# Optimization experiments

Measured on AMD Instinct MI355X. Metric: run time of the kernel, lower is better.

## Reference

```python
import jax, jax.numpy as jnp
import numpy as np

LEVELS = 6
_S = float(1.0 / np.sqrt(2.0))  # forward transform scales kernels by 1/sqrt(2)
# Complex Daubechies 6-tap filters (real, imag), pre-scaled for the forward DWT.
LO_R = [v * _S for v in (-0.0662912607, 0.1104854346, 0.6629126074, 0.6629126074, 0.1104854346, -0.0662912607)]
LO_I = [v * _S for v in (-0.0855816496, -0.0855816496, 0.1711632992, 0.1711632992, -0.0855816496, -0.0855816496)]
HI_R = [v * _S for v in (-0.0662912607, -0.1104854346, 0.6629126074, -0.6629126074, 0.1104854346, 0.0662912607)]
HI_I = [v * _S for v in (0.0855816496, -0.0855816496, -0.1711632992, 0.1711632992, 0.0855816496, -0.0855816496)]


def _corr_down(v, k):
    """Circular-padded 6-tap correlation along last axis, stride-2 decimation.
    v: [..., L] (L even) -> [..., L//2]. Matches torch: circular pad 3 each side,
    valid conv (L+1 outputs), then slice 0:-1:2."""
    L = v.shape[-1]
    vp = jnp.concatenate([v[..., -3:], v, v[..., :3]], axis=-1)  # [..., L+6]
    out = k[0] * vp[..., 0:L - 1:2]
    for t in range(1, 6):
        out = out + k[t] * vp[..., t:t + L - 1:2]
    return out


def _cconv_down(xr, xi, kr, ki):
    """Complex conv + downsample: (xr + i*xi) * (kr + i*ki) along last axis."""
    return (_corr_down(xr, kr) - _corr_down(xi, ki),
            _corr_down(xr, ki) + _corr_down(xi, kr))


def _decompose(xr, xi):
    """One DWT level. xr, xi: [B, C, h, w] -> (zr, zi) same shape."""
    # vertical pass: convolve along h (transpose so h is last)
    xrT = xr.swapaxes(-1, -2)  # [B, C, w, h]
    xiT = xi.swapaxes(-1, -2)
    lr, li = _cconv_down(xrT, xiT, LO_R, LO_I)  # [B, C, w, h//2]
    hr, hi = _cconv_down(xrT, xiT, HI_R, HI_I)
    yr = jnp.concatenate([lr, hr], axis=-1).swapaxes(-1, -2)  # [B, C, h, w]
    yi = jnp.concatenate([li, hi], axis=-1).swapaxes(-1, -2)
    # horizontal pass: convolve along w
    lr, li = _cconv_down(yr, yi, LO_R, LO_I)  # [B, C, h, w//2]
    hr, hi = _cconv_down(yr, yi, HI_R, HI_I)
    zr = jnp.concatenate([lr, hr], axis=-1)
    zi = jnp.concatenate([li, hi], axis=-1)
    return zr, zi


def setup_inputs() -> dict:
    key = jax.random.key(0)
    images = jax.random.uniform(key, (8, 3, 1024, 1024), dtype=jnp.float32)
    return {"images": images}


def reference(images):
    B, C, H, W = images.shape
    xr = images
    xi = jnp.zeros_like(images)
    res_r = jnp.zeros((B, C, H, W), images.dtype)
    res_i = jnp.zeros((B, C, H, W), images.dtype)
    for i in range(LEVELS):
        h, w = H >> i, W >> i
        if i == 0:
            sr, si = xr, xi
        else:
            sr, si = res_r[..., :h, :w], res_i[..., :h, :w]
        dr, di = _decompose(sr, si)
        res_r = res_r.at[..., :h, :w].set(dr)
        res_i = res_i.at[..., :h, :w].set(di)
    return jnp.stack([res_r, res_i], axis=2)  # [B, C, 2, H, W]
```

## Files before the change

kernel.cpp:

```cpp
#include <hip/hip_runtime.h>


#define SQ2 0.7071067811865476

constexpr float kLOR0 = (float)(-0.0662912607 * SQ2);
constexpr float kLOR1 = (float)( 0.1104854346 * SQ2);
constexpr float kLOR2 = (float)( 0.6629126074 * SQ2);
constexpr float kLOI0 = (float)(-0.0855816496 * SQ2);
constexpr float kLOI1 = (float)(-0.0855816496 * SQ2);
constexpr float kLOI2 = (float)( 0.1711632992 * SQ2);
constexpr float kHIR0 = (float)(-0.0662912607 * SQ2);
constexpr float kHIR1 = (float)(-0.1104854346 * SQ2);
constexpr float kHIR2 = (float)( 0.6629126074 * SQ2);
constexpr float kHII0 = (float)( 0.0855816496 * SQ2);
constexpr float kHII1 = (float)(-0.0855816496 * SQ2);
constexpr float kHII2 = (float)(-0.1711632992 * SQ2);

typedef float f2v __attribute__((ext_vector_type(2)));

__device__ __forceinline__ void band6(const float* xr, const float* xi,
                                      float& plr, float& pli, float& phr,
                                      float& phi) {
  const float s0 = xr[0] + xr[5], s1 = xr[1] + xr[4], s2 = xr[2] + xr[3];
  const float d0 = xr[0] - xr[5], d1 = xr[1] - xr[4], d2 = xr[2] - xr[3];
  const float t0 = xi[0] + xi[5], t1 = xi[1] + xi[4], t2 = xi[2] + xi[3];
  const float e0 = xi[0] - xi[5], e1 = xi[1] - xi[4], e2 = xi[2] - xi[3];
  plr = (kLOR0 * s0 + kLOR1 * s1 + kLOR2 * s2) -
        (kLOI0 * t0 + kLOI1 * t1 + kLOI2 * t2);
  pli = (kLOI0 * s0 + kLOI1 * s1 + kLOI2 * s2) +
        (kLOR0 * t0 + kLOR1 * t1 + kLOR2 * t2);
  phr = (kHIR0 * d0 + kHIR1 * d1 + kHIR2 * d2) -
        (kHII0 * e0 + kHII1 * e1 + kHII2 * e2);
  phi = (kHII0 * d0 + kHII1 * d1 + kHII2 * d2) +
        (kHIR0 * e0 + kHIR1 * e1 + kHIR2 * e2);
}

template <int TB, bool HAS_IMAG, bool LL_TO_WS>
__global__ __launch_bounds__(256) void dwt_kernel(
    const float* __restrict__ inR, const float* __restrict__ inI,
    float* __restrict__ out, float* __restrict__ llR, float* __restrict__ llI,
    int h, int w, int tilesPerRow, int tilesPerPlane, int cpx8, int HW,
    int W0) {
  constexpr int RROWS = 2 * TB + 4;
  constexpr int F4PR = TB / 2 + 2;
  constexpr int SW = 4 * F4PR;
  constexpr int NF4 = RROWS * F4PR;
  constexpr int NF4P = ((NF4 + 255) / 256) * 256;
  constexpr int YW = 2 * TB + 5;
  constexpr int HB = TB / 2;

  __shared__ float4 s4R[NF4P];
  __shared__ float4 s4I[HAS_IMAG ? NF4P : 1];
  __shared__ float yLR[HB * YW], yLI[HB * YW], yHR[HB * YW], yHI[HB * YW];

  const int tid = threadIdx.x;
  int bid = (int)blockIdx.x;
  bid = (bid & 7) * cpx8 + (bid >> 3);
  const int plane = bid / tilesPerPlane;
  const int trem = bid - plane * tilesPerPlane;
  const int ti = trem / tilesPerRow;
  const int tj = trem - ti * tilesPerRow;

  const int hm = h - 1;
  const int w4 = w >> 2, w4m = w4 - 1;
  const int rowstart = 2 * TB * ti - 3;
  const int col4start = HB * tj - 1;

  const float* pinR = inR + (size_t)plane * h * w;
  const float* pinI = HAS_IMAG ? (inI + (size_t)plane * h * w) : nullptr;

  {
    const int lane = tid & 63;
    const int wid = tid >> 6;
    for (int c0 = wid * 64; c0 < NF4P; c0 += 256) {
      const int idx = c0 + lane;
      const int r = idx / F4PR;
      const int q = idx - r * F4PR;
      const int gr = (rowstart + r) & hm;
      const int gq = (col4start + q) & w4m;
      const size_t goff = (size_t)gr * w4 + gq;
      __builtin_amdgcn_global_load_lds(
          (__attribute__((address_space(1))) void*)((const float4*)pinR + goff),
          (__attribute__((address_space(3))) void*)(&s4R[c0]), 16, 0, 0);
      if (HAS_IMAG) {
        __builtin_amdgcn_global_load_lds(
            (__attribute__((address_space(1))) void*)((const float4*)pinI + goff),
            (__attribute__((address_space(3))) void*)(&s4I[c0]), 16, 0, 0);
      }
    }
  }
  __syncthreads();

  const float* sRf = (const float*)s4R;
  const float* sIf = (const float*)s4I;
  const int i0 = TB * ti, j0g = TB * tj;
  const int h2 = h >> 1, w2 = w >> 1;
  float* outR = out + (size_t)plane * 2 * HW;
  float* outI = outR + HW;

#pragma unroll
  for (int p = 0; p < 2; ++p) {
    for (int idx = tid; idx < HB * YW; idx += 256) {
      const int il = idx / YW;
      const int c = idx - il * YW;
      const int rb = 2 * (p * HB + il);
      const float* col = sRf + rb * SW + c;
      const float x0 = col[0], x1 = col[SW], x2 = col[2 * SW];
      const float x3 = col[3 * SW], x4 = col[4 * SW], x5 = col[5 * SW];
      const float sr0 = x0 + x5, sr1 = x1 + x4, sr2 = x2 + x3;
      const float dr0 = x0 - x5, dr1 = x1 - x4, dr2 = x2 - x3;
      float lr = kLOR0 * sr0 + kLOR1 * sr1 + kLOR2 * sr2;
      float li = kLOI0 * sr0 + kLOI1 * sr1 + kLOI2 * sr2;
      float hr = kHIR0 * dr0 + kHIR1 * dr1 + kHIR2 * dr2;
      float hi = kHII0 * dr0 + kHII1 * dr1 + kHII2 * dr2;
      if (HAS_IMAG) {
        const float* colI = sIf + rb * SW + c;
        const float z0 = colI[0], z1 = colI[SW], z2 = colI[2 * SW];
        const float z3 = colI[3 * SW], z4 = colI[4 * SW], z5 = colI[5 * SW];
        const float si0 = z0 + z5, si1 = z1 + z4, si2 = z2 + z3;
        const float di0 = z0 - z5, di1 = z1 - z4, di2 = z2 - z3;
        lr -= kLOI0 * si0 + kLOI1 * si1 + kLOI2 * si2;
        li += kLOR0 * si0 + kLOR1 * si1 + kLOR2 * si2;
        hr -= kHII0 * di0 + kHII1 * di1 + kHII2 * di2;
        hi += kHIR0 * di0 + kHIR1 * di1 + kHIR2 * di2;
      }
      yLR[idx] = lr;
      yLI[idx] = li;
      yHR[idx] = hr;
      yHI[idx] = hi;
    }
    __syncthreads();

    constexpr int NJQ = TB / 2;
    const int jq = tid & (NJQ - 1);
    const int il = tid / NJQ;
    if (il < HB) {
      float o[8][2];
#pragma unroll
      for (int u = 0; u < 2; ++u) {
        const int cb = il * YW + 4 * jq + 2 * u + 1;
        band6(&yLR[cb], &yLI[cb], o[0][u], o[1][u], o[2][u], o[3][u]);
        band6(&yHR[cb], &yHI[cb], o[4][u], o[5][u], o[6][u], o[7][u]);
      }
      const int gi = i0 + p * HB + il;
      const int gj = j0g + 2 * jq;
      const int rlo = gi, rhi = h2 + gi, clo = gj, chi = w2 + gj;
      auto st = [&](float* pdst, int v) {
        f2v t;
        t.x = o[v][0];
        t.y = o[v][1];
        __builtin_nontemporal_store(t, (f2v*)pdst);
      };
      st(outR + (size_t)rlo * W0 + chi, 2);
      st(outI + (size_t)rlo * W0 + chi, 3);
      st(outR + (size_t)rhi * W0 + clo, 4);
      st(outI + (size_t)rhi * W0 + clo, 5);
      st(outR + (size_t)rhi * W0 + chi, 6);
      st(outI + (size_t)rhi * W0 + chi, 7);
      if (LL_TO_WS) {
        const size_t off = (size_t)plane * h2 * w2 + (size_t)gi * w2 + gj;
        f2v a, b;
        a.x = o[0][0];
        a.y = o[0][1];
        b.x = o[1][0];
        b.y = o[1][1];
        *(f2v*)(llR + off) = a;
        *(f2v*)(llI + off) = b;
      } else {
        st(outR + (size_t)rlo * W0 + clo, 0);
        st(outI + (size_t)rlo * W0 + clo, 1);
      }
    }
    __syncthreads();
  }
}

extern "C" void kernel_launch(void* const* d_in, const int* in_sizes, int n_in,
                              void* d_out, int out_size, void* d_ws,
                              size_t ws_size, hipStream_t stream) {
  const float* images = (const float*)d_in[0];
  float* out = (float*)d_out;
  constexpr int B = 8, C = 3, H = 1024, W = 1024, LEVELS = 6;

  float* wsf = (float*)d_ws;
  const size_t S0 = (size_t)B * C * 512 * 512;
  const size_t S1 = (size_t)B * C * 256 * 256;
  float* buf0R = wsf;
  float* buf0I = wsf + S0;
  float* buf1R = wsf + 2 * S0;
  float* buf1I = wsf + 2 * S0 + S1;

  const float* curR = images;
  const float* curI = nullptr;

  for (int lvl = 0; lvl < LEVELS; ++lvl) {
    const int h = H >> lvl, w = W >> lvl;
    const int TBl = (lvl == 5) ? 16 : 32;
    const int tpr = (w / 2) / TBl;
    const int tpp = tpr * tpr;
    const int grid = B * C * tpp;
    const int cpx8 = grid / 8;
    float* llR = (lvl & 1) ? buf1R : buf0R;
    float* llI = (lvl & 1) ? buf1I : buf0I;

    if (lvl == 0) {
      dwt_kernel<32, false, true><<<grid, 256, 0, stream>>>(
          curR, nullptr, out, llR, llI, h, w, tpr, tpp, cpx8, H * W, W);
    } else if (lvl < LEVELS - 1) {
      dwt_kernel<32, true, true><<<grid, 256, 0, stream>>>(
          curR, curI, out, llR, llI, h, w, tpr, tpp, cpx8, H * W, W);
    } else {
      dwt_kernel<16, true, false><<<grid, 256, 0, stream>>>(
          curR, curI, out, nullptr, nullptr, h, w, tpr, tpp, cpx8, H * W, W);
    }
    curR = llR;
    curI = llI;
  }
}
```

Measured before the change: 99.58 us.

## Fuse last three DWT levels into one per-plane tail kernel; vectorize LDS reads

Replaces the three separate launches for the small levels (128, 64, 32) with one tail kernel where each block handles one plane and loops over all three levels and their tiles. Intermediate LL data goes through workspace between levels. This removes launch and tail-latency overhead for the small grids. It also pads the intermediate LDS rows so the horizontal pass loads its inputs with aligned float4 reads instead of scalar LDS reads. The cost is that the tail runs only 24 blocks, each doing serial work, which leaves the GPU mostly idle for that phase. Within a block, data is passed between levels through global memory, relying on __syncthreads for visibility.

```diff
diff --git a/kernel.cpp b/kernel.cpp
--- a/kernel.cpp
+++ b/kernel.cpp
@@ -35,6 +35,12 @@
         (kHIR0 * e0 + kHIR1 * e1 + kHIR2 * e2);
 }
 
+__device__ __forceinline__ void gload16(const float4* src, float4* ldsDst) {
+  __builtin_amdgcn_global_load_lds(
+      (__attribute__((address_space(1))) const void*)src,
+      (__attribute__((address_space(3))) void*)ldsDst, 16, 0, 0);
+}
+
 template <int TB, bool HAS_IMAG, bool LL_TO_WS>
 __global__ __launch_bounds__(256) void dwt_kernel(
     const float* __restrict__ inR, const float* __restrict__ inI,
@@ -46,12 +52,15 @@
   constexpr int SW = 4 * F4PR;
   constexpr int NF4 = RROWS * F4PR;
   constexpr int NF4P = ((NF4 + 255) / 256) * 256;
-  constexpr int YW = 2 * TB + 5;
+  constexpr int YW = 2 * TB + 8;
+  constexpr int C2 = 2 * TB + 4;
   constexpr int HB = TB / 2;
+  constexpr int NJQ = TB / 2;
 
   __shared__ float4 s4R[NF4P];
   __shared__ float4 s4I[HAS_IMAG ? NF4P : 1];
-  __shared__ float yLR[HB * YW], yLI[HB * YW], yHR[HB * YW], yHI[HB * YW];
+  __shared__ __align__(16) float yLR[HB * YW], yLI[HB * YW];
+  __shared__ __align__(16) float yHR[HB * YW], yHI[HB * YW];
 
   const int tid = threadIdx.x;
   int bid = (int)blockIdx.x;
@@ -79,14 +88,8 @@
       const int gr = (rowstart + r) & hm;
       const int gq = (col4start + q) & w4m;
       const size_t goff = (size_t)gr * w4 + gq;
-      __builtin_amdgcn_global_load_lds(
-          (__attribute__((address_space(1))) void*)((const float4*)pinR + goff),
-          (__attribute__((address_space(3))) void*)(&s4R[c0]), 16, 0, 0);
-      if (HAS_IMAG) {
-        __builtin_amdgcn_global_load_lds(
-            (__attribute__((address_space(1))) void*)((const float4*)pinI + goff),
-            (__attribute__((address_space(3))) void*)(&s4I[c0]), 16, 0, 0);
-      }
+      gload16((const float4*)pinR + goff, &s4R[c0]);
+      if (HAS_IMAG) gload16((const float4*)pinI + goff, &s4I[c0]);
     }
   }
   __syncthreads();
@@ -100,11 +103,11 @@
 
 #pragma unroll
   for (int p = 0; p < 2; ++p) {
-    for (int idx = tid; idx < HB * YW; idx += 256) {
-      const int il = idx / YW;
-      const int c = idx - il * YW;
+    for (int idx = tid; idx < HB * C2; idx += 256) {
+      const int il = idx / C2;
+      const int c = idx - il * C2;
       const int rb = 2 * (p * HB + il);
-      const float* col = sRf + rb * SW + c;
+      const float* col = sRf + rb * SW + c + 1;
       const float x0 = col[0], x1 = col[SW], x2 = col[2 * SW];
       const float x3 = col[3 * SW], x4 = col[4 * SW], x5 = col[5 * SW];
       const float sr0 = x0 + x5, sr1 = x1 + x4, sr2 = x2 + x3;
@@ -114,7 +117,7 @@
       float hr = kHIR0 * dr0 + kHIR1 * dr1 + kHIR2 * dr2;
       float hi = kHII0 * dr0 + kHII1 * dr1 + kHII2 * dr2;
       if (HAS_IMAG) {
-        const float* colI = sIf + rb * SW + c;
+        const float* colI = sIf + rb * SW + c + 1;
         const float z0 = colI[0], z1 = colI[SW], z2 = colI[2 * SW];
         const float z3 = colI[3 * SW], z4 = colI[4 * SW], z5 = colI[5 * SW];
         const float si0 = z0 + z5, si1 = z1 + z4, si2 = z2 + z3;
@@ -124,23 +127,32 @@
         hr -= kHII0 * di0 + kHII1 * di1 + kHII2 * di2;
         hi += kHIR0 * di0 + kHIR1 * di1 + kHIR2 * di2;
       }
-      yLR[idx] = lr;
-      yLI[idx] = li;
-      yHR[idx] = hr;
-      yHI[idx] = hi;
+      const int yi = il * YW + c;
+      yLR[yi] = lr;
+      yLI[yi] = li;
+      yHR[yi] = hr;
+      yHI[yi] = hi;
     }
     __syncthreads();
 
-    constexpr int NJQ = TB / 2;
     const int jq = tid & (NJQ - 1);
     const int il = tid / NJQ;
     if (il < HB) {
+      const int base = il * YW + 4 * jq;
+      float xLR[8], xLI[8], xHR[8], xHI[8];
+      *(float4*)&xLR[0] = *(const float4*)&yLR[base];
+      *(float4*)&xLR[4] = *(const float4*)&yLR[base + 4];
+      *(float4*)&xLI[0] = *(const float4*)&yLI[base];
+      *(float4*)&xLI[4] = *(const float4*)&yLI[base + 4];
+      *(float4*)&xHR[0] = *(const float4*)&yHR[base];
+      *(float4*)&xHR[4] = *(const float4*)&yHR[base + 4];
+      *(float4*)&xHI[0] = *(const float4*)&yHI[base];
+      *(float4*)&xHI[4] = *(const float4*)&yHI[base + 4];
       float o[8][2];
 #pragma unroll
       for (int u = 0; u < 2; ++u) {
-        const int cb = il * YW + 4 * jq + 2 * u + 1;
-        band6(&yLR[cb], &yLI[cb], o[0][u], o[1][u], o[2][u], o[3][u]);
-        band6(&yHR[cb], &yHI[cb], o[4][u], o[5][u], o[6][u], o[7][u]);
+        band6(&xLR[2 * u], &xLI[2 * u], o[0][u], o[1][u], o[2][u], o[3][u]);
+        band6(&xHR[2 * u], &xHI[2 * u], o[4][u], o[5][u], o[6][u], o[7][u]);
       }
       const int gi = i0 + p * HB + il;
       const int gj = j0g + 2 * jq;
@@ -175,45 +187,207 @@
   }
 }
 
+__global__ __launch_bounds__(256) void dwt_tail_kernel(
+    const float* __restrict__ ws0R, const float* __restrict__ ws0I,
+    float* __restrict__ out, float* __restrict__ tmpAR,
+    float* __restrict__ tmpAI, float* __restrict__ tmpBR,
+    float* __restrict__ tmpBI, int HW, int W0) {
+  __shared__ float4 s4R[1280], s4I[1280];
+  __shared__ __align__(16) float yLR[16 * 72], yLI[16 * 72];
+  __shared__ __align__(16) float yHR[16 * 72], yHI[16 * 72];
+
+  const int tid = threadIdx.x;
+  const int plane = blockIdx.x;
+  float* outR = out + (size_t)plane * 2 * HW;
+  float* outI = outR + HW;
+
+  for (int lvl = 0; lvl < 3; ++lvl) {
+    const int h = 128 >> lvl;
+    const int TB = (lvl == 2) ? 16 : 32;
+    const int tpr = (h / 2) / TB;
+    const int ntiles = tpr * tpr;
+    const int HB = TB / 2;
+    const int F4PR = TB / 2 + 2;
+    const int SW = 4 * F4PR;
+    const int NF4 = (2 * TB + 4) * F4PR;
+    const int NF4P = ((NF4 + 255) / 256) * 256;
+    const int YW = 2 * TB + 8;
+    const int C2 = 2 * TB + 4;
+    const int hm = h - 1, w4 = h >> 2, w4m = w4 - 1;
+    const int h2 = h >> 1;
+    const bool llToOut = (lvl == 2);
+
+    const float* pinR;
+    const float* pinI;
+    float* plR = nullptr;
+    float* plI = nullptr;
+    if (lvl == 0) {
+      pinR = ws0R + (size_t)plane * 128 * 128;
+      pinI = ws0I + (size_t)plane * 128 * 128;
+      plR = tmpAR + (size_t)plane * 64 * 64;
+      plI = tmpAI + (size_t)plane * 64 * 64;
+    } else if (lvl == 1) {
+      pinR = tmpAR + (size_t)plane * 64 * 64;
+      pinI = tmpAI + (size_t)plane * 64 * 64;
+      plR = tmpBR + (size_t)plane * 32 * 32;
+      plI = tmpBI + (size_t)plane * 32 * 32;
+    } else {
+      pinR = tmpBR + (size_t)plane * 32 * 32;
+      pinI = tmpBI + (size_t)plane * 32 * 32;
+    }
+
+    for (int t = 0; t < ntiles; ++t) {
+      const int ti = t / tpr;
+      const int tj = t - ti * tpr;
+      const int rowstart = 2 * TB * ti - 3;
+      const int col4start = HB * tj - 1;
+
+      {
+        const int lane = tid & 63;
+        const int wid = tid >> 6;
+        for (int c0 = wid * 64; c0 < NF4P; c0 += 256) {
+          const int idx = c0 + lane;
+          const int r = idx / F4PR;
+          const int q = idx - r * F4PR;
+          const int gr = (rowstart + r) & hm;
+          const int gq = (col4start + q) & w4m;
+          const size_t goff = (size_t)gr * w4 + gq;
+          gload16((const float4*)pinR + goff, &s4R[c0]);
+          gload16((const float4*)pinI + goff, &s4I[c0]);
+        }
+      }
+      __syncthreads();
+
+      const float* sRf = (const float*)s4R;
+      const float* sIf = (const float*)s4I;
+      const int i0 = TB * ti, j0g = TB * tj;
+
+      for (int p = 0; p < 2; ++p) {
+        for (int idx = tid; idx < HB * C2; idx += 256) {
+          const int il = idx / C2;
+          const int c = idx - il * C2;
+          const int rb = 2 * (p * HB + il);
+          const float* col = sRf + rb * SW + c + 1;
+          const float* colI = sIf + rb * SW + c + 1;
+          const float x0 = col[0], x1 = col[SW], x2 = col[2 * SW];
+          const float x3 = col[3 * SW], x4 = col[4 * SW], x5 = col[5 * SW];
+          const float z0 = colI[0], z1 = colI[SW], z2 = colI[2 * SW];
+          const float z3 = colI[3 * SW], z4 = colI[4 * SW], z5 = colI[5 * SW];
+          const float sr0 = x0 + x5, sr1 = x1 + x4, sr2 = x2 + x3;
+          const float dr0 = x0 - x5, dr1 = x1 - x4, dr2 = x2 - x3;
+          const float si0 = z0 + z5, si1 = z1 + z4, si2 = z2 + z3;
+          const float di0 = z0 - z5, di1 = z1 - z4, di2 = z2 - z3;
+          const float lr = kLOR0 * sr0 + kLOR1 * sr1 + kLOR2 * sr2 -
+                           (kLOI0 * si0 + kLOI1 * si1 + kLOI2 * si2);
+          const float li = kLOI0 * sr0 + kLOI1 * sr1 + kLOI2 * sr2 +
+                           (kLOR0 * si0 + kLOR1 * si1 + kLOR2 * si2);
+          const float hr = kHIR0 * dr0 + kHIR1 * dr1 + kHIR2 * dr2 -
+                           (kHII0 * di0 + kHII1 * di1 + kHII2 * di2);
+          const float hi = kHII0 * dr0 + kHII1 * dr1 + kHII2 * dr2 +
+                           (kHIR0 * di0 + kHIR1 * di1 + kHIR2 * di2);
+          const int yi = il * YW + c;
+          yLR[yi] = lr;
+          yLI[yi] = li;
+          yHR[yi] = hr;
+          yHI[yi] = hi;
+        }
+        __syncthreads();
+
+        const int NJQ = TB / 2;
+        const int jq = tid & (NJQ - 1);
+        const int il = tid / NJQ;
+        if (il < HB) {
+          const int base = il * YW + 4 * jq;
+          float xLR[8], xLI[8], xHR[8], xHI[8];
+          *(float4*)&xLR[0] = *(const float4*)&yLR[base];
+          *(float4*)&xLR[4] = *(const float4*)&yLR[base + 4];
+          *(float4*)&xLI[0] = *(const float4*)&yLI[base];
+          *(float4*)&xLI[4] = *(const float4*)&yLI[base + 4];
+          *(float4*)&xHR[0] = *(const float4*)&yHR[base];
+          *(float4*)&xHR[4] = *(const float4*)&yHR[base + 4];
+          *(float4*)&xHI[0] = *(const float4*)&yHI[base];
+          *(float4*)&xHI[4] = *(const float4*)&yHI[base + 4];
+          float o[8][2];
+#pragma unroll
+          for (int u = 0; u < 2; ++u) {
+            band6(&xLR[2 * u], &xLI[2 * u], o[0][u], o[1][u], o[2][u],
+                  o[3][u]);
+            band6(&xHR[2 * u], &xHI[2 * u], o[4][u], o[5][u], o[6][u],
+                  o[7][u]);
+          }
+          const int gi = i0 + p * HB + il;
+          const int gj = j0g + 2 * jq;
+          const int rlo = gi, rhi = h2 + gi, clo = gj, chi = h2 + gj;
+          auto st = [&](float* pdst, int v) {
+            f2v tv;
+            tv.x = o[v][0];
+            tv.y = o[v][1];
+            __builtin_nontemporal_store(tv, (f2v*)pdst);
+          };
+          st(outR + (size_t)rlo * W0 + chi, 2);
+          st(outI + (size_t)rlo * W0 + chi, 3);
+          st(outR + (size_t)rhi * W0 + clo, 4);
+          st(outI + (size_t)rhi * W0 + clo, 5);
+          st(outR + (size_t)rhi * W0 + chi, 6);
+          st(outI + (size_t)rhi * W0 + chi, 7);
+          if (llToOut) {
+            st(outR + (size_t)rlo * W0 + clo, 0);
+            st(outI + (size_t)rlo * W0 + clo, 1);
+          } else {
+            const size_t off = (size_t)gi * h2 + gj;
+            f2v a, b;
+            a.x = o[0][0];
+            a.y = o[0][1];
+            b.x = o[1][0];
+            b.y = o[1][1];
+            *(f2v*)(plR + off) = a;
+            *(f2v*)(plI + off) = b;
+          }
+        }
+        __syncthreads();
+      }
+    }
+  }
+}
+
 extern "C" void kernel_launch(void* const* d_in, const int* in_sizes, int n_in,
                               void* d_out, int out_size, void* d_ws,
                               size_t ws_size, hipStream_t stream) {
   const float* images = (const float*)d_in[0];
   float* out = (float*)d_out;
-  constexpr int B = 8, C = 3, H = 1024, W = 1024, LEVELS = 6;
+  constexpr int B = 8, C = 3, H = 1024, W = 1024;
+  constexpr int NP = B * C;
 
   float* wsf = (float*)d_ws;
-  const size_t S0 = (size_t)B * C * 512 * 512;
-  const size_t S1 = (size_t)B * C * 256 * 256;
+  const size_t S0 = (size_t)NP * 512 * 512;
+  const size_t S1 = (size_t)NP * 256 * 256;
   float* buf0R = wsf;
   float* buf0I = wsf + S0;
   float* buf1R = wsf + 2 * S0;
   float* buf1I = wsf + 2 * S0 + S1;
-
-  const float* curR = images;
-  const float* curI = nullptr;
-
-  for (int lvl = 0; lvl < LEVELS; ++lvl) {
-    const int h = H >> lvl, w = W >> lvl;
-    const int TBl = (lvl == 5) ? 16 : 32;
-    const int tpr = (w / 2) / TBl;
-    const int tpp = tpr * tpr;
-    const int grid = B * C * tpp;
-    const int cpx8 = grid / 8;
-    float* llR = (lvl & 1) ? buf1R : buf0R;
-    float* llI = (lvl & 1) ? buf1I : buf0I;
-
-    if (lvl == 0) {
-      dwt_kernel<32, false, true><<<grid, 256, 0, stream>>>(
-          curR, nullptr, out, llR, llI, h, w, tpr, tpp, cpx8, H * W, W);
-    } else if (lvl < LEVELS - 1) {
-      dwt_kernel<32, true, true><<<grid, 256, 0, stream>>>(
-          curR, curI, out, llR, llI, h, w, tpr, tpp, cpx8, H * W, W);
-    } else {
-      dwt_kernel<16, true, false><<<grid, 256, 0, stream>>>(
-          curR, curI, out, nullptr, nullptr, h, w, tpr, tpp, cpx8, H * W, W);
-    }
-    curR = llR;
-    curI = llI;
-  }
-}
+  float* tmpAR = buf1R;
+  float* tmpAI = buf1I;
+  float* tmpBR = buf1R + (size_t)NP * 64 * 64;
+  float* tmpBI = buf1I + (size_t)NP * 64 * 64;
+
+  {
+    const int tpr = 512 / 32, tpp = tpr * tpr, grid = NP * tpp;
+    dwt_kernel<32, false, true><<<grid, 256, 0, stream>>>(
+        images, nullptr, out, buf0R, buf0I, 1024, 1024, tpr, tpp, grid / 8,
+        H * W, W);
+  }
+  {
+    const int tpr = 256 / 32, tpp = tpr * tpr, grid = NP * tpp;
+    dwt_kernel<32, true, true><<<grid, 256, 0, stream>>>(
+        buf0R, buf0I, out, buf1R, buf1I, 512, 512, tpr, tpp, grid / 8, H * W,
+        W);
+  }
+  {
+    const int tpr = 128 / 32, tpp = tpr * tpr, grid = NP * tpp;
+    dwt_kernel<32, true, true><<<grid, 256, 0, stream>>>(
+        buf1R, buf1I, out, buf0R, buf0I, 256, 256, tpr, tpp, grid / 8, H * W,
+        W);
+  }
+  dwt_tail_kernel<<<NP, 256, 0, stream>>>(buf0R, buf0I, out, tmpAR, tmpAI,
+                                          tmpBR, tmpBI, H * W, W);
+}
```

After: 109.7 us. 1.1x slower.
